# Performance work log

Hardware: AMD Instinct MI355X
Metric: run time of the kernel (lower is better)

The kernel has to match this reference:

```python
import jax, jax.numpy as jnp
import numpy as np

N_NODES = 100000
N_EDGES = 1600000
FEAT = 128
LAYERS = [128, 128, 64]


def setup_inputs() -> dict:
    key = jax.random.key(0)
    ks = jax.random.split(key, 10)
    x = jax.random.normal(ks[0], (N_NODES, FEAT), dtype=jnp.float32)
    edge_index = jax.random.randint(ks[1], (2, N_EDGES), 0, N_NODES, dtype=jnp.int32)
    edge_weight = jax.random.uniform(ks[2], (N_EDGES,), dtype=jnp.float32)
    # GCNConv params (glorot weights + zero bias)
    def glorot(k, fi, fo):
        s = jnp.sqrt(6.0 / (fi + fo)).astype(jnp.float32)
        return jax.random.uniform(k, (fi, fo), jnp.float32, -s, s)
    W1 = glorot(ks[3], FEAT, LAYERS[0]); b1 = jnp.zeros((LAYERS[0],), jnp.float32)
    W2 = glorot(ks[4], LAYERS[0], LAYERS[1]); b2 = jnp.zeros((LAYERS[1],), jnp.float32)
    W3 = glorot(ks[5], LAYERS[1], LAYERS[2]); b3 = jnp.zeros((LAYERS[2],), jnp.float32)
    return {"x": x, "edge_index": edge_index, "edge_weight": edge_weight,
            "W1": W1, "b1": b1, "W2": W2, "b2": b2, "W3": W3, "b3": b3}


def _gcn_norm(edge_index, edge_weight, n_nodes):
    # symmetric normalization, no self loops (add_self_loops=False)
    src, dst = edge_index[0], edge_index[1]
    deg = jax.ops.segment_sum(edge_weight, dst, num_segments=n_nodes)
    dinv = jnp.where(deg > 0, jax.lax.rsqrt(jnp.maximum(deg, 1e-30)), 0.0)
    return dinv[src] * edge_weight * dinv[dst]


def _gcn_conv(h, src, dst, norm, W, b, n_nodes):
    h = h @ W                                  # linear first (PyG GCNConv)
    msg = norm[:, None] * h[src]               # [E, out_dim] gather
    out = jax.ops.segment_sum(msg, dst, num_segments=n_nodes)
    return out + b


def reference(x, edge_index, edge_weight, W1, b1, W2, b2, W3, b3):
    n = x.shape[0]
    src, dst = edge_index[0], edge_index[1]
    norm = _gcn_norm(edge_index, edge_weight, n)
    h = _gcn_conv(x, src, dst, norm, W1, b1, n)
    h = jax.nn.relu(h)                          # dropout = identity (eval)
    h = _gcn_conv(h, src, dst, norm, W2, b2, n)
    h = jax.nn.relu(h)
    h = _gcn_conv(h, src, dst, norm, W3, b3, n)
    return (h, h)
```

## Files before the change

### kernel.cpp

```cpp
#include <hip/hip_runtime.h>
#include <hip/hip_bf16.h>
#include <stdint.h>

#define N_NODES 100000
#define N_EDGES 1600000
#define NB_P 400
#define EPP 4000
#define NBUCK 391

typedef __bf16 bf16x8 __attribute__((ext_vector_type(8)));
typedef float f32x4 __attribute__((ext_vector_type(4)));
typedef unsigned short u16;

__device__ __forceinline__ u16 f2b(float f) {
    uint32_t u = __builtin_bit_cast(uint32_t, f);
    uint32_t r = (u + 0x7fffu + ((u >> 16) & 1u)) >> 16;
    return (u16)r;
}
__device__ __forceinline__ float b2f(uint32_t lo16) {
    return __builtin_bit_cast(float, lo16 << 16);
}

__global__ __launch_bounds__(256) void part_hist(const int* __restrict__ dstp,
                                                 int* __restrict__ hist) {
    __shared__ int h[NBUCK];
    int t = threadIdx.x, p = blockIdx.x;
    for (int b = t; b < NBUCK; b += 256) h[b] = 0;
    __syncthreads();
    int e0 = p * EPP;
    for (int i = t; i < EPP; i += 256)
        atomicAdd(&h[dstp[e0 + i] >> 8], 1);
    __syncthreads();
    for (int b = t; b < NBUCK; b += 256) hist[b * NB_P + p] = h[b];
}

__global__ void bucket_totals(const int* __restrict__ hist, int* __restrict__ totals) {
    int w = (blockIdx.x * 256 + threadIdx.x) >> 6;
    if (w >= NBUCK) return;
    int lane = threadIdx.x & 63;
    int s = 0;
    for (int p = lane; p < NB_P; p += 64) s += hist[w * NB_P + p];
    #pragma unroll
    for (int off = 32; off; off >>= 1) s += __shfl_down(s, off, 64);
    if (lane == 0) totals[w] = s;
}

__global__ void bucket_scan(const int* __restrict__ totals, int* __restrict__ base,
                            int* __restrict__ rowptr) {
    int lane = threadIdx.x;
    int carry = 0;
    for (int s0 = 0; s0 < NBUCK; s0 += 64) {
        int b = s0 + lane;
        int v = (b < NBUCK) ? totals[b] : 0;
        int x = v;
        #pragma unroll
        for (int off = 1; off < 64; off <<= 1) {
            int y = __shfl_up(x, off, 64);
            if (lane >= off) x += y;
        }
        if (b < NBUCK) base[b] = carry + x - v;
        carry += __shfl(x, 63, 64);
    }
    if (lane == 0) { base[NBUCK] = carry; rowptr[N_NODES] = carry; }
}

__global__ void bucket_off(const int* __restrict__ hist, const int* __restrict__ base,
                           int* __restrict__ off) {
    int w = (blockIdx.x * 256 + threadIdx.x) >> 6;
    if (w >= NBUCK) return;
    int lane = threadIdx.x & 63;
    int run = base[w];
    for (int s0 = 0; s0 < NB_P; s0 += 64) {
        int p = s0 + lane;
        int v = (p < NB_P) ? hist[w * NB_P + p] : 0;
        int x = v;
        #pragma unroll
        for (int o = 1; o < 64; o <<= 1) {
            int y = __shfl_up(x, o, 64);
            if (lane >= o) x += y;
        }
        if (p < NB_P) off[w * NB_P + p] = run + x - v;
        run += __shfl(x, 63, 64);
    }
}

__global__ __launch_bounds__(256) void part_scatter(const int* __restrict__ srcp,
                                                    const int* __restrict__ dstp,
                                                    const float* __restrict__ ew,
                                                    const int* __restrict__ off,
                                                    int4* __restrict__ part) {
    __shared__ int cur[NBUCK];
    int t = threadIdx.x, p = blockIdx.x;
    for (int b = t; b < NBUCK; b += 256) cur[b] = off[b * NB_P + p];
    __syncthreads();
    int e0 = p * EPP;
    for (int i = t; i < EPP; i += 256) {
        int e = e0 + i;
        int s = srcp[e], d = dstp[e];
        float w = ew[e];
        int pos = atomicAdd(&cur[d >> 8], 1);
        int4 E;
        E.x = s; E.y = d; E.z = __float_as_int(w); E.w = 0;
        part[pos] = E;
    }
}

__global__ __launch_bounds__(256) void bucket_build(const int4* __restrict__ part,
                                                    const int* __restrict__ base,
                                                    int* __restrict__ rowptr,
                                                    float* __restrict__ dinv,
                                                    int2* __restrict__ csr) {
    __shared__ int h[256];
    __shared__ float dw[256];
    __shared__ int cur[256];
    __shared__ int wsum[4];
    int t = threadIdx.x, b = blockIdx.x;
    h[t] = 0; dw[t] = 0.f;
    __syncthreads();
    int jb = base[b], je = base[b + 1];
    for (int i = jb + t; i < je; i += 256) {
        int4 E = part[i];
        int li = E.y & 255;
        atomicAdd(&h[li], 1);
        atomicAdd(&dw[li], __int_as_float(E.z));
    }
    __syncthreads();
    int lane = t & 63, wid = t >> 6;
    int v = h[t];
    int x = v;
    #pragma unroll
    for (int o = 1; o < 64; o <<= 1) {
        int y = __shfl_up(x, o, 64);
        if (lane >= o) x += y;
    }
    if (lane == 63) wsum[wid] = x;
    __syncthreads();
    int woff = 0;
    for (int j = 0; j < wid; j++) woff += wsum[j];
    int excl = jb + woff + x - v;
    int node = b * 256 + t;
    if (node < N_NODES) {
        rowptr[node] = excl;
        float s = dw[t];
        dinv[node] = (s > 0.f) ? rsqrtf(fmaxf(s, 1e-30f)) : 0.f;
    }
    cur[t] = excl;
    __syncthreads();
    for (int i = jb + t; i < je; i += 256) {
        int4 E = part[i];
        int li = E.y & 255;
        int pos = atomicAdd(&cur[li], 1);
        int2 c;
        c.x = E.x; c.y = E.z;
        csr[pos] = c;
    }
}

__global__ void wconv_all(const float* __restrict__ W1, const float* __restrict__ W2,
                          const float* __restrict__ W3, u16* __restrict__ Wt1,
                          u16* __restrict__ Wt2, u16* __restrict__ Wt3) {
    int i = blockIdx.x * 256 + threadIdx.x;
    if (i < 16384) {
        int k = i >> 7, n = i & 127;
        Wt1[n * 128 + k] = f2b(W1[i]);
    } else if (i < 32768) {
        int j = i - 16384;
        int k = j >> 7, n = j & 127;
        Wt2[n * 128 + k] = f2b(W2[j]);
    } else if (i < 40960) {
        int j = i - 32768;
        int k = j >> 6, n = j & 63;
        Wt3[n * 128 + k] = f2b(W3[j]);
    }
}

__global__ __launch_bounds__(256) void gemm_f32A(const float* __restrict__ A,
                                                 const u16* __restrict__ Bt,
                                                 const float* __restrict__ dinv,
                                                 u16* __restrict__ C, int Dout) {
    int wid = (blockIdx.x * 256 + threadIdx.x) >> 6;
    if (wid >= N_NODES / 16) return;
    int lane = threadIdx.x & 63;
    int m = lane & 15;
    int k0 = (lane >> 4) * 8;
    int r0 = wid * 16;
    const float* ap = A + (size_t)(r0 + m) * 128 + k0;
    bf16x8 a[4];
    #pragma unroll
    for (int q = 0; q < 4; q++) {
        float4 lo = *(const float4*)(ap + q * 32);
        float4 hi = *(const float4*)(ap + q * 32 + 4);
        union { u16 s[8]; bf16x8 v; } u_;
        u_.s[0] = f2b(lo.x); u_.s[1] = f2b(lo.y); u_.s[2] = f2b(lo.z); u_.s[3] = f2b(lo.w);
        u_.s[4] = f2b(hi.x); u_.s[5] = f2b(hi.y); u_.s[6] = f2b(hi.z); u_.s[7] = f2b(hi.w);
        a[q] = u_.v;
    }
    int ntiles = Dout >> 4;
    int rbase = r0 + ((lane >> 4) << 2);
    float dv[4];
    #pragma unroll
    for (int i2 = 0; i2 < 4; i2++) dv[i2] = dinv[rbase + i2];
    for (int tn = 0; tn < ntiles; tn++) {
        const u16* bp = Bt + (size_t)(tn * 16 + m) * 128 + k0;
        f32x4 acc = {0.f, 0.f, 0.f, 0.f};
        acc = __builtin_amdgcn_mfma_f32_16x16x32_bf16(a[0], *(const bf16x8*)(bp + 0),  acc, 0, 0, 0);
        acc = __builtin_amdgcn_mfma_f32_16x16x32_bf16(a[1], *(const bf16x8*)(bp + 32), acc, 0, 0, 0);
        acc = __builtin_amdgcn_mfma_f32_16x16x32_bf16(a[2], *(const bf16x8*)(bp + 64), acc, 0, 0, 0);
        acc = __builtin_amdgcn_mfma_f32_16x16x32_bf16(a[3], *(const bf16x8*)(bp + 96), acc, 0, 0, 0);
        int col = tn * 16 + m;
        #pragma unroll
        for (int i2 = 0; i2 < 4; i2++)
            C[(size_t)(rbase + i2) * Dout + col] = f2b(acc[i2] * dv[i2]);
    }
}

__global__ __launch_bounds__(256) void gemm_bf16(const u16* __restrict__ A,
                                                 const u16* __restrict__ Bt,
                                                 const float* __restrict__ dinv,
                                                 u16* __restrict__ C, int Dout) {
    int wid = (blockIdx.x * 256 + threadIdx.x) >> 6;
    if (wid >= N_NODES / 16) return;
    int lane = threadIdx.x & 63;
    int m = lane & 15;
    int k0 = (lane >> 4) * 8;
    int r0 = wid * 16;
    const u16* ap = A + (size_t)(r0 + m) * 128 + k0;
    bf16x8 a0 = *(const bf16x8*)(ap + 0);
    bf16x8 a1 = *(const bf16x8*)(ap + 32);
    bf16x8 a2 = *(const bf16x8*)(ap + 64);
    bf16x8 a3 = *(const bf16x8*)(ap + 96);
    int ntiles = Dout >> 4;
    int rbase = r0 + ((lane >> 4) << 2);
    float dv[4];
    #pragma unroll
    for (int i2 = 0; i2 < 4; i2++) dv[i2] = dinv[rbase + i2];
    for (int tn = 0; tn < ntiles; tn++) {
        const u16* bp = Bt + (size_t)(tn * 16 + m) * 128 + k0;
        f32x4 acc = {0.f, 0.f, 0.f, 0.f};
        acc = __builtin_amdgcn_mfma_f32_16x16x32_bf16(a0, *(const bf16x8*)(bp + 0),  acc, 0, 0, 0);
        acc = __builtin_amdgcn_mfma_f32_16x16x32_bf16(a1, *(const bf16x8*)(bp + 32), acc, 0, 0, 0);
        acc = __builtin_amdgcn_mfma_f32_16x16x32_bf16(a2, *(const bf16x8*)(bp + 64), acc, 0, 0, 0);
        acc = __builtin_amdgcn_mfma_f32_16x16x32_bf16(a3, *(const bf16x8*)(bp + 96), acc, 0, 0, 0);
        int col = tn * 16 + m;
        #pragma unroll
        for (int i2 = 0; i2 < 4; i2++)
            C[(size_t)(rbase + i2) * Dout + col] = f2b(acc[i2] * dv[i2]);
    }
}

__global__ __launch_bounds__(256) void agg128(const u16* __restrict__ H,
                                              const int* __restrict__ row_ptr,
                                              const int2* __restrict__ csr,
                                              const float* __restrict__ dinv,
                                              const float* __restrict__ bias,
                                              u16* __restrict__ out, int do_relu) {
    int node = (blockIdx.x * 256 + threadIdx.x) >> 6;
    if (node >= N_NODES) return;
    int lane = threadIdx.x & 63;
    int c = lane * 2;
    float a0 = 0.f, a1 = 0.f;
    int jb = row_ptr[node], je = row_ptr[node + 1];
    for (int base = jb; base < je; base += 64) {
        int n = je - base;
        if (n > 64) n = 64;
        int2 meta;
        if (base + lane < je) meta = csr[base + lane];
        else { meta.x = 0; meta.y = 0; }
        for (int e = 0; e < n; e += 8) {
            int s[8]; float w[8];
            #pragma unroll
            for (int u = 0; u < 8; u++) {
                int idx = e + u;
                int sv = __shfl(meta.x, idx, 64);
                int wv = __shfl(meta.y, idx, 64);
                bool ok = idx < n;
                s[u] = ok ? sv : 0;
                w[u] = ok ? __int_as_float(wv) : 0.f;
            }
            uint32_t p[8];
            #pragma unroll
            for (int u = 0; u < 8; u++)
                p[u] = *(const uint32_t*)(H + (size_t)s[u] * 128 + c);
            #pragma unroll
            for (int u = 0; u < 8; u++) {
                a0 += w[u] * b2f(p[u] & 0xffffu);
                a1 += w[u] * b2f(p[u] >> 16);
            }
        }
    }
    float dv = dinv[node];
    a0 = dv * a0 + bias[c];
    a1 = dv * a1 + bias[c + 1];
    if (do_relu) { a0 = fmaxf(a0, 0.f); a1 = fmaxf(a1, 0.f); }
    uint32_t o = (uint32_t)f2b(a0) | ((uint32_t)f2b(a1) << 16);
    *(uint32_t*)(out + (size_t)node * 128 + c) = o;
}

__global__ __launch_bounds__(256) void agg64_out(const u16* __restrict__ H,
                                                 const int* __restrict__ row_ptr,
                                                 const int2* __restrict__ csr,
                                                 const float* __restrict__ dinv,
                                                 const float* __restrict__ bias,
                                                 float* __restrict__ out) {
    int wv = (blockIdx.x * 256 + threadIdx.x) >> 6;
    int node = wv * 2 + ((threadIdx.x >> 5) & 1);
    if (node >= N_NODES) return;
    int lane = threadIdx.x & 31;
    int c = lane * 2;
    float a0 = 0.f, a1 = 0.f;
    int jb = row_ptr[node], je = row_ptr[node + 1];
    for (int base = jb; base < je; base += 32) {
        int n = je - base;
        if (n > 32) n = 32;
        int2 meta;
        if (base + lane < je) meta = csr[base + lane];
        else { meta.x = 0; meta.y = 0; }
        for (int e = 0; e < n; e += 8) {
            int s[8]; float w[8];
            #pragma unroll
            for (int u = 0; u < 8; u++) {
                int idx = e + u;
                int sv = __shfl(meta.x, idx, 32);
                int wv2 = __shfl(meta.y, idx, 32);
                bool ok = idx < n;
                s[u] = ok ? sv : 0;
                w[u] = ok ? __int_as_float(wv2) : 0.f;
            }
            uint32_t p[8];
            #pragma unroll
            for (int u = 0; u < 8; u++)
                p[u] = *(const uint32_t*)(H + (size_t)s[u] * 64 + c);
            #pragma unroll
            for (int u = 0; u < 8; u++) {
                a0 += w[u] * b2f(p[u] & 0xffffu);
                a1 += w[u] * b2f(p[u] >> 16);
            }
        }
    }
    float dv = dinv[node];
    a0 = dv * a0 + bias[c];
    a1 = dv * a1 + bias[c + 1];
    size_t o = (size_t)node * 64 + c;
    float2 r; r.x = a0; r.y = a1;
    *(float2*)(out + o) = r;
    *(float2*)(out + (size_t)N_NODES * 64 + o) = r;
}

extern "C" void kernel_launch(void* const* d_in, const int* in_sizes, int n_in,
                              void* d_out, int out_size, void* d_ws, size_t ws_size,
                              hipStream_t stream) {
    const float* x  = (const float*)d_in[0];
    const int* eidx = (const int*)d_in[1];
    const float* ew = (const float*)d_in[2];
    const float* W1 = (const float*)d_in[3];
    const float* b1 = (const float*)d_in[4];
    const float* W2 = (const float*)d_in[5];
    const float* b2 = (const float*)d_in[6];
    const float* W3 = (const float*)d_in[7];
    const float* b3 = (const float*)d_in[8];
    const int* srcp = eidx;
    const int* dstp = eidx + N_EDGES;

    char* ws = (char*)d_ws;
    size_t off_ = 0;
    auto alloc = [&](size_t bytes) -> void* {
        void* p = ws + off_;
        off_ += (bytes + 255) & ~(size_t)255;
        return p;
    };
    int*   hist   = (int*)  alloc((size_t)NBUCK * NB_P * 4);
    int*   offm   = (int*)  alloc((size_t)NBUCK * NB_P * 4);
    int*   totals = (int*)  alloc((size_t)NBUCK * 4);
    int*   base   = (int*)  alloc((size_t)(NBUCK + 1) * 4);
    int*   rowptr = (int*)  alloc((size_t)(N_NODES + 1) * 4);
    int2*  csr    = (int2*) alloc((size_t)N_EDGES * 8);
    float* dinv   = (float*)alloc((size_t)N_NODES * 4);
    u16*   Wt1    = (u16*)  alloc(128 * 128 * 2);
    u16*   Wt2    = (u16*)  alloc(128 * 128 * 2);
    u16*   Wt3    = (u16*)  alloc(128 * 64 * 2);
    u16*   bufA   = (u16*)  alloc((size_t)N_NODES * 128 * 2);
    u16*   bufB   = (u16*)  alloc((size_t)N_NODES * 128 * 2);
    int4*  part   = (int4*)bufA;

    part_hist<<<NB_P, 256, 0, stream>>>(dstp, hist);
    bucket_totals<<<(NBUCK + 3) / 4, 256, 0, stream>>>(hist, totals);
    bucket_scan<<<1, 64, 0, stream>>>(totals, base, rowptr);
    bucket_off<<<(NBUCK + 3) / 4, 256, 0, stream>>>(hist, base, offm);
    part_scatter<<<NB_P, 256, 0, stream>>>(srcp, dstp, ew, offm, part);
    bucket_build<<<NBUCK, 256, 0, stream>>>(part, base, rowptr, dinv, csr);
    wconv_all<<<160, 256, 0, stream>>>(W1, W2, W3, Wt1, Wt2, Wt3);

    int gemm_blocks = (N_NODES / 16 + 3) / 4;
    gemm_f32A<<<gemm_blocks, 256, 0, stream>>>(x, Wt1, dinv, bufA, 128);
    agg128<<<N_NODES / 4, 256, 0, stream>>>(bufA, rowptr, csr, dinv, b1, bufB, 1);
    gemm_bf16<<<gemm_blocks, 256, 0, stream>>>(bufB, Wt2, dinv, bufA, 128);
    agg128<<<N_NODES / 4, 256, 0, stream>>>(bufA, rowptr, csr, dinv, b2, bufB, 1);
    gemm_bf16<<<gemm_blocks, 256, 0, stream>>>(bufB, Wt3, dinv, bufA, 64);
    agg64_out<<<N_NODES / 8, 256, 0, stream>>>(bufA, rowptr, csr, dinv, b3, (float*)d_out);
}
```

Measured before the change: 422.3 us.

## Split edges across lane groups with wide vector gathers in aggregation kernels

The aggregation kernels now split each wavefront into four 16-lane groups. Each group handles a different edge and gathers 16-byte (or 8-byte) feature chunks per lane, where before every lane walked every edge with 4-byte loads. The goal is more gathers in flight and fewer load instructions per edge. Edge metadata is staged through LDS instead of shuffles, and the four partial sums are combined with xor-shuffles at the end. The 64-wide output kernel moves from two nodes per wave to one, which may leave lanes idle on low-degree nodes and adds reduction overhead.

```diff
diff --git a/kernel.cpp b/kernel.cpp
--- a/kernel.cpp
+++ b/kernel.cpp
@@ -17,8 +17,11 @@
     uint32_t r = (u + 0x7fffu + ((u >> 16) & 1u)) >> 16;
     return (u16)r;
 }
-__device__ __forceinline__ float b2f(uint32_t lo16) {
-    return __builtin_bit_cast(float, lo16 << 16);
+__device__ __forceinline__ float blo(uint32_t p) {
+    return __builtin_bit_cast(float, p << 16);
+}
+__device__ __forceinline__ float bhi(uint32_t p) {
+    return __builtin_bit_cast(float, p & 0xffff0000u);
 }
 
 __global__ __launch_bounds__(256) void part_hist(const int* __restrict__ dstp,
@@ -254,46 +257,65 @@
                                               const float* __restrict__ dinv,
                                               const float* __restrict__ bias,
                                               u16* __restrict__ out, int do_relu) {
-    int node = (blockIdx.x * 256 + threadIdx.x) >> 6;
+    __shared__ int2 ms_all[4][64];
+    int wslot = threadIdx.x >> 6;
+    int node = blockIdx.x * 4 + wslot;
     if (node >= N_NODES) return;
     int lane = threadIdx.x & 63;
-    int c = lane * 2;
-    float a0 = 0.f, a1 = 0.f;
+    int grp = lane >> 4;
+    int li = lane & 15;
+    int2* ms = ms_all[wslot];
+    float4 bia = *(const float4*)(bias + 8 * li);
+    float4 bib = *(const float4*)(bias + 8 * li + 4);
+    float acc[8] = {0.f, 0.f, 0.f, 0.f, 0.f, 0.f, 0.f, 0.f};
     int jb = row_ptr[node], je = row_ptr[node + 1];
     for (int base = jb; base < je; base += 64) {
         int n = je - base;
         if (n > 64) n = 64;
-        int2 meta;
-        if (base + lane < je) meta = csr[base + lane];
-        else { meta.x = 0; meta.y = 0; }
-        for (int e = 0; e < n; e += 8) {
-            int s[8]; float w[8];
+        int2 m;
+        if (base + lane < je) m = csr[base + lane];
+        else { m.x = 0; m.y = 0; }
+        ms[lane] = m;
+        for (int e = 0; e < n; e += 16) {
+            uint4 p[4]; float w[4];
             #pragma unroll
-            for (int u = 0; u < 8; u++) {
-                int idx = e + u;
-                int sv = __shfl(meta.x, idx, 64);
-                int wv = __shfl(meta.y, idx, 64);
-                bool ok = idx < n;
-                s[u] = ok ? sv : 0;
-                w[u] = ok ? __int_as_float(wv) : 0.f;
+            for (int q = 0; q < 4; q++) {
+                int2 mm = ms[(e + q * 4 + grp) & 63];
+                w[q] = __int_as_float(mm.y);
+                p[q] = *(const uint4*)(H + (size_t)mm.x * 128 + li * 8);
             }
-            uint32_t p[8];
             #pragma unroll
-            for (int u = 0; u < 8; u++)
-                p[u] = *(const uint32_t*)(H + (size_t)s[u] * 128 + c);
-            #pragma unroll
-            for (int u = 0; u < 8; u++) {
-                a0 += w[u] * b2f(p[u] & 0xffffu);
-                a1 += w[u] * b2f(p[u] >> 16);
+            for (int q = 0; q < 4; q++) {
+                acc[0] += w[q] * blo(p[q].x); acc[1] += w[q] * bhi(p[q].x);
+                acc[2] += w[q] * blo(p[q].y); acc[3] += w[q] * bhi(p[q].y);
+                acc[4] += w[q] * blo(p[q].z); acc[5] += w[q] * bhi(p[q].z);
+                acc[6] += w[q] * blo(p[q].w); acc[7] += w[q] * bhi(p[q].w);
             }
         }
     }
-    float dv = dinv[node];
-    a0 = dv * a0 + bias[c];
-    a1 = dv * a1 + bias[c + 1];
-    if (do_relu) { a0 = fmaxf(a0, 0.f); a1 = fmaxf(a1, 0.f); }
-    uint32_t o = (uint32_t)f2b(a0) | ((uint32_t)f2b(a1) << 16);
-    *(uint32_t*)(out + (size_t)node * 128 + c) = o;
+    #pragma unroll
+    for (int d = 0; d < 8; d++) {
+        acc[d] += __shfl_xor(acc[d], 16, 64);
+        acc[d] += __shfl_xor(acc[d], 32, 64);
+    }
+    if (lane < 16) {
+        float dv = dinv[node];
+        float r[8];
+        r[0] = fmaf(dv, acc[0], bia.x); r[1] = fmaf(dv, acc[1], bia.y);
+        r[2] = fmaf(dv, acc[2], bia.z); r[3] = fmaf(dv, acc[3], bia.w);
+        r[4] = fmaf(dv, acc[4], bib.x); r[5] = fmaf(dv, acc[5], bib.y);
+        r[6] = fmaf(dv, acc[6], bib.z); r[7] = fmaf(dv, acc[7], bib.w);
+        if (do_relu) {
+            #pragma unroll
+            for (int d = 0; d < 8; d++) r[d] = fmaxf(r[d], 0.f);
+        }
+        uint4 st;
+        st.x = (uint32_t)f2b(r[0]) | ((uint32_t)f2b(r[1]) << 16);
+        st.y = (uint32_t)f2b(r[2]) | ((uint32_t)f2b(r[3]) << 16);
+        st.z = (uint32_t)f2b(r[4]) | ((uint32_t)f2b(r[5]) << 16);
+        st.w = (uint32_t)f2b(r[6]) | ((uint32_t)f2b(r[7]) << 16);
+        *(uint4*)(out + (size_t)node * 128 + li * 8) = st;
+    }
 }
 
 __global__ __launch_bounds__(256) void agg64_out(const u16* __restrict__ H,
@@ -302,48 +324,55 @@
                                                  const float* __restrict__ dinv,
                                                  const float* __restrict__ bias,
                                                  float* __restrict__ out) {
-    int wv = (blockIdx.x * 256 + threadIdx.x) >> 6;
-    int node = wv * 2 + ((threadIdx.x >> 5) & 1);
+    __shared__ int2 ms_all[4][64];
+    int wslot = threadIdx.x >> 6;
+    int node = blockIdx.x * 4 + wslot;
     if (node >= N_NODES) return;
-    int lane = threadIdx.x & 31;
-    int c = lane * 2;
-    float a0 = 0.f, a1 = 0.f;
+    int lane = threadIdx.x & 63;
+    int grp = lane >> 4;
+    int li = lane & 15;
+    int2* ms = ms_all[wslot];
+    float4 bi = *(const float4*)(bias + 4 * li);
+    float acc[4] = {0.f, 0.f, 0.f, 0.f};
     int jb = row_ptr[node], je = row_ptr[node + 1];
-    for (int base = jb; base < je; base += 32) {
+    for (int base = jb; base < je; base += 64) {
         int n = je - base;
-        if (n > 32) n = 32;
-        int2 meta;
-        if (base + lane < je) meta = csr[base + lane];
-        else { meta.x = 0; meta.y = 0; }
-        for (int e = 0; e < n; e += 8) {
-            int s[8]; float w[8];
+        if (n > 64) n = 64;
+        int2 m;
+        if (base + lane < je) m = csr[base + lane];
+        else { m.x = 0; m.y = 0; }
+        ms[lane] = m;
+        for (int e = 0; e < n; e += 16) {
+            uint2 p[4]; float w[4];
             #pragma unroll
-            for (int u = 0; u < 8; u++) {
-                int idx = e + u;
-                int sv = __shfl(meta.x, idx, 32);
-                int wv2 = __shfl(meta.y, idx, 32);
-                bool ok = idx < n;
-                s[u] = ok ? sv : 0;
-                w[u] = ok ? __int_as_float(wv2) : 0.f;
+            for (int q = 0; q < 4; q++) {
+                int2 mm = ms[(e + q * 4 + grp) & 63];
+                w[q] = __int_as_float(mm.y);
+                p[q] = *(const uint2*)(H + (size_t)mm.x * 64 + li * 4);
             }
-            uint32_t p[8];
             #pragma unroll
-            for (int u = 0; u < 8; u++)
-                p[u] = *(const uint32_t*)(H + (size_t)s[u] * 64 + c);
-            #pragma unroll
-            for (int u = 0; u < 8; u++) {
-                a0 += w[u] * b2f(p[u] & 0xffffu);
-                a1 += w[u] * b2f(p[u] >> 16);
+            for (int q = 0; q < 4; q++) {
+                acc[0] += w[q] * blo(p[q].x); acc[1] += w[q] * bhi(p[q].x);
+                acc[2] += w[q] * blo(p[q].y); acc[3] += w[q] * bhi(p[q].y);
             }
         }
     }
-    float dv = dinv[node];
-    a0 = dv * a0 + bias[c];
-    a1 = dv * a1 + bias[c + 1];
-    size_t o = (size_t)node * 64 + c;
-    float2 r; r.x = a0; r.y = a1;
-    *(float2*)(out + o) = r;
-    *(float2*)(out + (size_t)N_NODES * 64 + o) = r;
+    #pragma unroll
+    for (int d = 0; d < 4; d++) {
+        acc[d] += __shfl_xor(acc[d], 16, 64);
+        acc[d] += __shfl_xor(acc[d], 32, 64);
+    }
+    if (lane < 16) {
+        float dv = dinv[node];
+        float4 r;
+        r.x = fmaf(dv, acc[0], bi.x);
+        r.y = fmaf(dv, acc[1], bi.y);
+        r.z = fmaf(dv, acc[2], bi.z);
+        r.w = fmaf(dv, acc[3], bi.w);
+        size_t o = (size_t)node * 64 + li * 4;
+        *(float4*)(out + o) = r;
+        *(float4*)(out + (size_t)N_NODES * 64 + o) = r;
+    }
 }
 
 extern "C" void kernel_launch(void* const* d_in, const int* in_sizes, int n_in,
@@ -396,5 +425,5 @@
     gemm_bf16<<<gemm_blocks, 256, 0, stream>>>(bufB, Wt2, dinv, bufA, 128);
     agg128<<<N_NODES / 4, 256, 0, stream>>>(bufA, rowptr, csr, dinv, b2, bufB, 1);
     gemm_bf16<<<gemm_blocks, 256, 0, stream>>>(bufB, Wt3, dinv, bufA, 64);
-    agg64_out<<<N_NODES / 8, 256, 0, stream>>>(bufA, rowptr, csr, dinv, b3, (float*)d_out);
-}
+    agg64_out<<<N_NODES / 4, 256, 0, stream>>>(bufA, rowptr, csr, dinv, b3, (float*)d_out);
+}
```

Result: slower. 435.0 us (+3.0%).

## Slice feature buffers into 16-column planes and pack CSR edges into 32 bits

Applied to the files above, without the earlier changes.

Intermediate feature matrices are stored as 16-column slices, one plane per slice, so each aggregation block gathers 32-byte rows from a smaller working set that fits in cache better. Blocks are split per slice, and each wave processes 8 edges at once with 8 lanes per edge, then reduces with cross-lane shuffles. CSR entries become one 32-bit word holding a 17-bit source index and a 15-bit bf16 weight (sign bit dropped, valid since weights are non-negative), which halves metadata traffic. The cost is lower weight precision, metadata re-read once per slice (8x for 128-wide layers), more blocks, and a shuffle reduction tail.

```diff
diff --git a/kernel.cpp b/kernel.cpp
--- a/kernel.cpp
+++ b/kernel.cpp
@@ -17,8 +17,14 @@
     uint32_t r = (u + 0x7fffu + ((u >> 16) & 1u)) >> 16;
     return (u16)r;
 }
-__device__ __forceinline__ float b2f(uint32_t lo16) {
-    return __builtin_bit_cast(float, lo16 << 16);
+__device__ __forceinline__ float blo(uint32_t p) {
+    return __builtin_bit_cast(float, p << 16);
+}
+__device__ __forceinline__ float bhi(uint32_t p) {
+    return __builtin_bit_cast(float, p & 0xffff0000u);
+}
+__device__ __forceinline__ float wdec(uint32_t m) {
+    return __builtin_bit_cast(float, (m & 0x7fffu) << 16);
 }
 
 __global__ __launch_bounds__(256) void part_hist(const int* __restrict__ dstp,
@@ -109,7 +115,7 @@
                                                     const int* __restrict__ base,
                                                     int* __restrict__ rowptr,
                                                     float* __restrict__ dinv,
-                                                    int2* __restrict__ csr) {
+                                                    uint32_t* __restrict__ meta) {
     __shared__ int h[256];
     __shared__ float dw[256];
     __shared__ int cur[256];
@@ -150,9 +156,7 @@
         int4 E = part[i];
         int li = E.y & 255;
         int pos = atomicAdd(&cur[li], 1);
-        int2 c;
-        c.x = E.x; c.y = E.z;
-        csr[pos] = c;
+        meta[pos] = ((uint32_t)E.x << 15) | (uint32_t)f2b(__int_as_float(E.z));
     }
 }
 
@@ -174,10 +178,11 @@
     }
 }
 
+
 __global__ __launch_bounds__(256) void gemm_f32A(const float* __restrict__ A,
                                                  const u16* __restrict__ Bt,
                                                  const float* __restrict__ dinv,
-                                                 u16* __restrict__ C, int Dout) {
+                                                 u16* __restrict__ Cs, int Dout) {
     int wid = (blockIdx.x * 256 + threadIdx.x) >> 6;
     if (wid >= N_NODES / 16) return;
     int lane = threadIdx.x & 63;
@@ -207,28 +212,28 @@
         acc = __builtin_amdgcn_mfma_f32_16x16x32_bf16(a[1], *(const bf16x8*)(bp + 32), acc, 0, 0, 0);
         acc = __builtin_amdgcn_mfma_f32_16x16x32_bf16(a[2], *(const bf16x8*)(bp + 64), acc, 0, 0, 0);
         acc = __builtin_amdgcn_mfma_f32_16x16x32_bf16(a[3], *(const bf16x8*)(bp + 96), acc, 0, 0, 0);
-        int col = tn * 16 + m;
         #pragma unroll
         for (int i2 = 0; i2 < 4; i2++)
-            C[(size_t)(rbase + i2) * Dout + col] = f2b(acc[i2] * dv[i2]);
+            Cs[((size_t)tn * N_NODES + rbase + i2) * 16 + m] = f2b(acc[i2] * dv[i2]);
     }
 }
 
 __global__ __launch_bounds__(256) void gemm_bf16(const u16* __restrict__ A,
                                                  const u16* __restrict__ Bt,
                                                  const float* __restrict__ dinv,
-                                                 u16* __restrict__ C, int Dout) {
+                                                 u16* __restrict__ Cs, int Dout) {
     int wid = (blockIdx.x * 256 + threadIdx.x) >> 6;
     if (wid >= N_NODES / 16) return;
     int lane = threadIdx.x & 63;
     int m = lane & 15;
     int k0 = (lane >> 4) * 8;
     int r0 = wid * 16;
-    const u16* ap = A + (size_t)(r0 + m) * 128 + k0;
-    bf16x8 a0 = *(const bf16x8*)(ap + 0);
-    bf16x8 a1 = *(const bf16x8*)(ap + 32);
-    bf16x8 a2 = *(const bf16x8*)(ap + 64);
-    bf16x8 a3 = *(const bf16x8*)(ap + 96);
+    const u16* arow = A + (size_t)(r0 + m) * 16 + (k0 & 8) + (size_t)(k0 >> 4) * N_NODES * 16;
+    const size_t sstep = (size_t)2 * N_NODES * 16;
+    bf16x8 a0 = *(const bf16x8*)(arow);
+    bf16x8 a1 = *(const bf16x8*)(arow + sstep);
+    bf16x8 a2 = *(const bf16x8*)(arow + 2 * sstep);
+    bf16x8 a3 = *(const bf16x8*)(arow + 3 * sstep);
     int ntiles = Dout >> 4;
     int rbase = r0 + ((lane >> 4) << 2);
     float dv[4];
@@ -241,109 +246,91 @@
         acc = __builtin_amdgcn_mfma_f32_16x16x32_bf16(a1, *(const bf16x8*)(bp + 32), acc, 0, 0, 0);
         acc = __builtin_amdgcn_mfma_f32_16x16x32_bf16(a2, *(const bf16x8*)(bp + 64), acc, 0, 0, 0);
         acc = __builtin_amdgcn_mfma_f32_16x16x32_bf16(a3, *(const bf16x8*)(bp + 96), acc, 0, 0, 0);
-        int col = tn * 16 + m;
         #pragma unroll
         for (int i2 = 0; i2 < 4; i2++)
-            C[(size_t)(rbase + i2) * Dout + col] = f2b(acc[i2] * dv[i2]);
-    }
-}
-
-__global__ __launch_bounds__(256) void agg128(const u16* __restrict__ H,
+            Cs[((size_t)tn * N_NODES + rbase + i2) * 16 + m] = f2b(acc[i2] * dv[i2]);
+    }
+}
+
+__global__ __launch_bounds__(256) void agg128s(const u16* __restrict__ Hs,
+                                               const int* __restrict__ row_ptr,
+                                               const uint32_t* __restrict__ meta,
+                                               const float* __restrict__ dinv,
+                                               const float* __restrict__ bias,
+                                               u16* __restrict__ outs, int do_relu) {
+    int slice = blockIdx.x & 7;
+    int node = (blockIdx.x >> 3) * 4 + (threadIdx.x >> 6);
+    int lane = threadIdx.x & 63;
+    int epos = lane >> 3;
+    int li = lane & 7;
+    const u16* Hsl = Hs + (size_t)slice * N_NODES * 16;
+    float a0 = 0.f, a1 = 0.f;
+    int jb = row_ptr[node], je = row_ptr[node + 1];
+    for (int base = jb; base < je; base += 16) {
+        int i0 = base + epos, i1 = base + 8 + epos;
+        uint32_t m0 = meta[min(i0, je - 1)];
+        uint32_t m1 = meta[min(i1, je - 1)];
+        float w0 = (i0 < je) ? wdec(m0) : 0.f;
+        float w1 = (i1 < je) ? wdec(m1) : 0.f;
+        uint32_t p0 = *(const uint32_t*)(Hsl + (size_t)(m0 >> 15) * 16 + li * 2);
+        uint32_t p1 = *(const uint32_t*)(Hsl + (size_t)(m1 >> 15) * 16 + li * 2);
+        a0 += w0 * blo(p0); a1 += w0 * bhi(p0);
+        a0 += w1 * blo(p1); a1 += w1 * bhi(p1);
+    }
+    a0 += __shfl_xor(a0, 8, 64);  a1 += __shfl_xor(a1, 8, 64);
+    a0 += __shfl_xor(a0, 16, 64); a1 += __shfl_xor(a1, 16, 64);
+    a0 += __shfl_xor(a0, 32, 64); a1 += __shfl_xor(a1, 32, 64);
+    if (lane < 8) {
+        float dv = dinv[node];
+        int c = slice * 16 + li * 2;
+        float2 bi = *(const float2*)(bias + c);
+        float r0 = fmaf(dv, a0, bi.x);
+        float r1 = fmaf(dv, a1, bi.y);
+        if (do_relu) { r0 = fmaxf(r0, 0.f); r1 = fmaxf(r1, 0.f); }
+        uint32_t o = (uint32_t)f2b(r0) | ((uint32_t)f2b(r1) << 16);
+        *(uint32_t*)(outs + ((size_t)slice * N_NODES + node) * 16 + li * 2) = o;
+    }
+}
+
+__global__ __launch_bounds__(256) void agg64s(const u16* __restrict__ Hs,
                                               const int* __restrict__ row_ptr,
-                                              const int2* __restrict__ csr,
+                                              const uint32_t* __restrict__ meta,
                                               const float* __restrict__ dinv,
                                               const float* __restrict__ bias,
-                                              u16* __restrict__ out, int do_relu) {
-    int node = (blockIdx.x * 256 + threadIdx.x) >> 6;
-    if (node >= N_NODES) return;
-    int lane = threadIdx.x & 63;
-    int c = lane * 2;
+                                              float* __restrict__ out) {
+    int slice = blockIdx.x & 3;
+    int node = (blockIdx.x >> 2) * 4 + (threadIdx.x >> 6);
+    int lane = threadIdx.x & 63;
+    int epos = lane >> 3;
+    int li = lane & 7;
+    const u16* Hsl = Hs + (size_t)slice * N_NODES * 16;
     float a0 = 0.f, a1 = 0.f;
     int jb = row_ptr[node], je = row_ptr[node + 1];
-    for (int base = jb; base < je; base += 64) {
-        int n = je - base;
-        if (n > 64) n = 64;
-        int2 meta;
-        if (base + lane < je) meta = csr[base + lane];
-        else { meta.x = 0; meta.y = 0; }
-        for (int e = 0; e < n; e += 8) {
-            int s[8]; float w[8];
-            #pragma unroll
-            for (int u = 0; u < 8; u++) {
-                int idx = e + u;
-                int sv = __shfl(meta.x, idx, 64);
-                int wv = __shfl(meta.y, idx, 64);
-                bool ok = idx < n;
-                s[u] = ok ? sv : 0;
-                w[u] = ok ? __int_as_float(wv) : 0.f;
-            }
-            uint32_t p[8];
-            #pragma unroll
-            for (int u = 0; u < 8; u++)
-                p[u] = *(const uint32_t*)(H + (size_t)s[u] * 128 + c);
-            #pragma unroll
-            for (int u = 0; u < 8; u++) {
-                a0 += w[u] * b2f(p[u] & 0xffffu);
-                a1 += w[u] * b2f(p[u] >> 16);
-            }
-        }
-    }
-    float dv = dinv[node];
-    a0 = dv * a0 + bias[c];
-    a1 = dv * a1 + bias[c + 1];
-    if (do_relu) { a0 = fmaxf(a0, 0.f); a1 = fmaxf(a1, 0.f); }
-    uint32_t o = (uint32_t)f2b(a0) | ((uint32_t)f2b(a1) << 16);
-    *(uint32_t*)(out + (size_t)node * 128 + c) = o;
-}
-
-__global__ __launch_bounds__(256) void agg64_out(const u16* __restrict__ H,
-                                                 const int* __restrict__ row_ptr,
-                                                 const int2* __restrict__ csr,
-                                                 const float* __restrict__ dinv,
-                                                 const float* __restrict__ bias,
-                                                 float* __restrict__ out) {
-    int wv = (blockIdx.x * 256 + threadIdx.x) >> 6;
-    int node = wv * 2 + ((threadIdx.x >> 5) & 1);
-    if (node >= N_NODES) return;
-    int lane = threadIdx.x & 31;
-    int c = lane * 2;
-    float a0 = 0.f, a1 = 0.f;
-    int jb = row_ptr[node], je = row_ptr[node + 1];
-    for (int base = jb; base < je; base += 32) {
-        int n = je - base;
-        if (n > 32) n = 32;
-        int2 meta;
-        if (base + lane < je) meta = csr[base + lane];
-        else { meta.x = 0; meta.y = 0; }
-        for (int e = 0; e < n; e += 8) {
-            int s[8]; float w[8];
-            #pragma unroll
-            for (int u = 0; u < 8; u++) {
-                int idx = e + u;
-                int sv = __shfl(meta.x, idx, 32);
-                int wv2 = __shfl(meta.y, idx, 32);
-                bool ok = idx < n;
-                s[u] = ok ? sv : 0;
-                w[u] = ok ? __int_as_float(wv2) : 0.f;
-            }
-            uint32_t p[8];
-            #pragma unroll
-            for (int u = 0; u < 8; u++)
-                p[u] = *(const uint32_t*)(H + (size_t)s[u] * 64 + c);
-            #pragma unroll
-            for (int u = 0; u < 8; u++) {
-                a0 += w[u] * b2f(p[u] & 0xffffu);
-                a1 += w[u] * b2f(p[u] >> 16);
-            }
-        }
-    }
-    float dv = dinv[node];
-    a0 = dv * a0 + bias[c];
-    a1 = dv * a1 + bias[c + 1];
-    size_t o = (size_t)node * 64 + c;
-    float2 r; r.x = a0; r.y = a1;
-    *(float2*)(out + o) = r;
-    *(float2*)(out + (size_t)N_NODES * 64 + o) = r;
+    for (int base = jb; base < je; base += 16) {
+        int i0 = base + epos, i1 = base + 8 + epos;
+        uint32_t m0 = meta[min(i0, je - 1)];
+        uint32_t m1 = meta[min(i1, je - 1)];
+        float w0 = (i0 < je) ? wdec(m0) : 0.f;
+        float w1 = (i1 < je) ? wdec(m1) : 0.f;
+        uint32_t p0 = *(const uint32_t*)(Hsl + (size_t)(m0 >> 15) * 16 + li * 2);
+        uint32_t p1 = *(const uint32_t*)(Hsl + (size_t)(m1 >> 15) * 16 + li * 2);
+        a0 += w0 * blo(p0); a1 += w0 * bhi(p0);
+        a0 += w1 * blo(p1); a1 += w1 * bhi(p1);
+    }
+    a0 += __shfl_xor(a0, 8, 64);  a1 += __shfl_xor(a1, 8, 64);
+    a0 += __shfl_xor(a0, 16, 64); a1 += __shfl_xor(a1, 16, 64);
+    a0 += __shfl_xor(a0, 32, 64); a1 += __shfl_xor(a1, 32, 64);
+    if (lane < 8) {
+        float dv = dinv[node];
+        int c = slice * 16 + li * 2;
+        float2 bi = *(const float2*)(bias + c);
+        float2 r;
+        r.x = fmaf(dv, a0, bi.x);
+        r.y = fmaf(dv, a1, bi.y);
+        size_t o = (size_t)node * 64 + c;
+        *(float2*)(out + o) = r;
+        *(float2*)(out + (size_t)N_NODES * 64 + o) = r;
+    }
 }
 
 extern "C" void kernel_launch(void* const* d_in, const int* in_sizes, int n_in,
@@ -368,33 +355,33 @@
         off_ += (bytes + 255) & ~(size_t)255;
         return p;
     };
-    int*   hist   = (int*)  alloc((size_t)NBUCK * NB_P * 4);
-    int*   offm   = (int*)  alloc((size_t)NBUCK * NB_P * 4);
-    int*   totals = (int*)  alloc((size_t)NBUCK * 4);
-    int*   base   = (int*)  alloc((size_t)(NBUCK + 1) * 4);
-    int*   rowptr = (int*)  alloc((size_t)(N_NODES + 1) * 4);
-    int2*  csr    = (int2*) alloc((size_t)N_EDGES * 8);
-    float* dinv   = (float*)alloc((size_t)N_NODES * 4);
-    u16*   Wt1    = (u16*)  alloc(128 * 128 * 2);
-    u16*   Wt2    = (u16*)  alloc(128 * 128 * 2);
-    u16*   Wt3    = (u16*)  alloc(128 * 64 * 2);
-    u16*   bufA   = (u16*)  alloc((size_t)N_NODES * 128 * 2);
-    u16*   bufB   = (u16*)  alloc((size_t)N_NODES * 128 * 2);
-    int4*  part   = (int4*)bufA;
+    int*      hist   = (int*)     alloc((size_t)NBUCK * NB_P * 4);
+    int*      offm   = (int*)     alloc((size_t)NBUCK * NB_P * 4);
+    int*      totals = (int*)     alloc((size_t)NBUCK * 4);
+    int*      base   = (int*)     alloc((size_t)(NBUCK + 1) * 4);
+    int*      rowptr = (int*)     alloc((size_t)(N_NODES + 1) * 4);
+    uint32_t* meta   = (uint32_t*)alloc((size_t)N_EDGES * 4);
+    float*    dinv   = (float*)   alloc((size_t)N_NODES * 4);
+    u16*      Wt1    = (u16*)     alloc(128 * 128 * 2);
+    u16*      Wt2    = (u16*)     alloc(128 * 128 * 2);
+    u16*      Wt3    = (u16*)     alloc(128 * 64 * 2);
+    u16*      bufA   = (u16*)     alloc((size_t)N_NODES * 128 * 2);
+    u16*      bufB   = (u16*)     alloc((size_t)N_NODES * 128 * 2);
+    int4*     part   = (int4*)bufA;
 
     part_hist<<<NB_P, 256, 0, stream>>>(dstp, hist);
     bucket_totals<<<(NBUCK + 3) / 4, 256, 0, stream>>>(hist, totals);
     bucket_scan<<<1, 64, 0, stream>>>(totals, base, rowptr);
     bucket_off<<<(NBUCK + 3) / 4, 256, 0, stream>>>(hist, base, offm);
     part_scatter<<<NB_P, 256, 0, stream>>>(srcp, dstp, ew, offm, part);
-    bucket_build<<<NBUCK, 256, 0, stream>>>(part, base, rowptr, dinv, csr);
+    bucket_build<<<NBUCK, 256, 0, stream>>>(part, base, rowptr, dinv, meta);
     wconv_all<<<160, 256, 0, stream>>>(W1, W2, W3, Wt1, Wt2, Wt3);
 
     int gemm_blocks = (N_NODES / 16 + 3) / 4;
     gemm_f32A<<<gemm_blocks, 256, 0, stream>>>(x, Wt1, dinv, bufA, 128);
-    agg128<<<N_NODES / 4, 256, 0, stream>>>(bufA, rowptr, csr, dinv, b1, bufB, 1);
+    agg128s<<<(N_NODES / 4) * 8, 256, 0, stream>>>(bufA, rowptr, meta, dinv, b1, bufB, 1);
     gemm_bf16<<<gemm_blocks, 256, 0, stream>>>(bufB, Wt2, dinv, bufA, 128);
-    agg128<<<N_NODES / 4, 256, 0, stream>>>(bufA, rowptr, csr, dinv, b2, bufB, 1);
+    agg128s<<<(N_NODES / 4) * 8, 256, 0, stream>>>(bufA, rowptr, meta, dinv, b2, bufB, 1);
     gemm_bf16<<<gemm_blocks, 256, 0, stream>>>(bufB, Wt3, dinv, bufA, 64);
-    agg64_out<<<N_NODES / 8, 256, 0, stream>>>(bufA, rowptr, csr, dinv, b3, (float*)d_out);
-}
+    agg64s<<<(N_NODES / 4) * 4, 256, 0, stream>>>(bufA, rowptr, meta, dinv, b3, (float*)d_out);
+}
```

Result: slower. 764.6 us (+81.1%).
